# Performance work log

Hardware: AMD Instinct MI355X
Metric: run time of the kernel (lower is better)

The kernel has to match this reference:

```python
import jax, jax.numpy as jnp
import numpy as np

EPS = 1e-06

def elu_feature_map(x):
    # elu(x) + 1, matching torch.nn.functional.elu default alpha=1
    return jax.nn.elu(x) + 1.0

def setup_inputs() -> dict:
    key = jax.random.key(0)
    k1, k2, k3 = jax.random.split(key, 3)
    n, L, h, e = 4, 8192, 8, 64
    queries = jax.random.normal(k1, (n, L, h, e), dtype=jnp.float32)
    keys = jax.random.normal(k2, (n, L, h, e), dtype=jnp.float32)
    values = jax.random.normal(k3, (n, L, h, e), dtype=jnp.float32)
    return {"queries": queries, "keys": keys, "values": values}

def reference(queries, keys, values):
    n, l, h, e = queries.shape
    softmax_temp = e ** (-0.25)
    q = elu_feature_map(queries * softmax_temp)   # [n, l, h, e]
    k = elu_feature_map(keys * softmax_temp)      # [n, s, h, e]
    # kv: sum over sequence of outer products k (x) v -> [n, h, d_v, e]
    kv = jnp.einsum('nshd,nshm->nhmd', k, values)
    # normalizer z = 1 / (q . sum_s k)
    z = 1.0 / (jnp.einsum('nlhd,nhd->nlh', q, k.sum(axis=1)) + EPS)
    v = jnp.einsum('nlhd,nhmd,nlh->nlhm', q, kv, z)
    return v
```

## Files before the change

kernel.cpp:

```cpp
#include <hip/hip_runtime.h>

#define N_      4
#define L_      8192
#define H_      8
#define E_      64
#define NH_     (N_ * H_)
#define STRIDE_ (H_ * E_)
#define SPLIT_  32
#define RPB_    (L_ / SPLIT_)
#define NKB_    (RPB_ / 32)
#define PITCH_  40

#define PKV_FLOATS ((size_t)NH_ * SPLIT_ * E_ * E_)
#define PKS_FLOATS ((size_t)NH_ * SPLIT_ * E_)
#define KVT_FLOATS ((size_t)NH_ * E_ * E_ / 2)
#define PKS_OFF  PKV_FLOATS
#define KVT_OFF  (PKV_FLOATS + PKS_FLOATS)
#define KSUM_OFF (KVT_OFF + KVT_FLOATS)

typedef short bf16x8 __attribute__((ext_vector_type(8)));
typedef float f32x16 __attribute__((ext_vector_type(16)));

__device__ __forceinline__ float featmap(float x) {
    float xs = x * 0.35355339059327373f;
    return xs > 0.0f ? xs + 1.0f : __expf(xs);
}
__device__ __forceinline__ unsigned short f2bf(float f) {
    union { float f; unsigned u; } c{f};
    unsigned r = c.u + 0x7FFFu + ((c.u >> 16) & 1u);
    return (unsigned short)(r >> 16);
}
__device__ __forceinline__ unsigned pack2(float lo, float hi) {
    return (unsigned)f2bf(lo) | ((unsigned)f2bf(hi) << 16);
}

__global__ __launch_bounds__(256) void la_kv(
    const float* __restrict__ keys, const float* __restrict__ values,
    float* __restrict__ pkv, float* __restrict__ pks)
{
    const int blk = blockIdx.x;
    const int nh = blk / SPLIT_, chunk = blk % SPLIT_;
    const int n = nh / H_, h = nh % H_;
    const int t = threadIdx.x, l = t & 63;
    const int w = t >> 6, wd = w >> 1, wm = w & 1;
    const int d4 = t & 15, p = t >> 4;
    const int lm = l & 31, lh = l >> 5;

    __shared__ unsigned short Kb[2][E_][PITCH_];
    __shared__ unsigned short Vb[2][E_][PITCH_];

    f32x16 acc = {0,0,0,0,0,0,0,0,0,0,0,0,0,0,0,0};
    float sk0 = 0.f, sk1 = 0.f, sk2 = 0.f, sk3 = 0.f;

    const size_t base = (size_t)n * (L_ * H_ * E_) + (size_t)h * E_;
    const float* kp = keys   + base + (size_t)(chunk * RPB_ + 2 * p) * STRIDE_ + d4 * 4;
    const float* vp = values + base + (size_t)(chunk * RPB_ + 2 * p) * STRIDE_ + d4 * 4;

    float4 k0 = *(const float4*)kp;
    float4 k1 = *(const float4*)(kp + STRIDE_);
    float4 v0 = *(const float4*)vp;
    float4 v1 = *(const float4*)(vp + STRIDE_);

    for (int i = 0; i < NKB_; ++i) {
        const int buf = i & 1;
        float4 nk0, nk1, nv0, nv1;
        if (i + 1 < NKB_) {
            kp += 32 * STRIDE_; vp += 32 * STRIDE_;
            nk0 = *(const float4*)kp; nk1 = *(const float4*)(kp + STRIDE_);
            nv0 = *(const float4*)vp; nv1 = *(const float4*)(vp + STRIDE_);
        } else { nk0 = k0; nk1 = k1; nv0 = v0; nv1 = v1; }

        const float a0 = featmap(k0.x), a1 = featmap(k0.y),
                    a2 = featmap(k0.z), a3 = featmap(k0.w);
        const float b0 = featmap(k1.x), b1 = featmap(k1.y),
                    b2 = featmap(k1.z), b3 = featmap(k1.w);
        sk0 += a0 + b0; sk1 += a1 + b1; sk2 += a2 + b2; sk3 += a3 + b3;

        *(unsigned*)&Kb[buf][4 * d4 + 0][2 * p] = pack2(a0, b0);
        *(unsigned*)&Kb[buf][4 * d4 + 1][2 * p] = pack2(a1, b1);
        *(unsigned*)&Kb[buf][4 * d4 + 2][2 * p] = pack2(a2, b2);
        *(unsigned*)&Kb[buf][4 * d4 + 3][2 * p] = pack2(a3, b3);
        *(unsigned*)&Vb[buf][4 * d4 + 0][2 * p] = pack2(v0.x, v1.x);
        *(unsigned*)&Vb[buf][4 * d4 + 1][2 * p] = pack2(v0.y, v1.y);
        *(unsigned*)&Vb[buf][4 * d4 + 2][2 * p] = pack2(v0.z, v1.z);
        *(unsigned*)&Vb[buf][4 * d4 + 3][2 * p] = pack2(v0.w, v1.w);

        __syncthreads();

        bf16x8 af0 = *(const bf16x8*)&Kb[buf][32 * wd + lm][8 * lh];
        bf16x8 bf0 = *(const bf16x8*)&Vb[buf][32 * wm + lm][8 * lh];
        acc = __builtin_amdgcn_mfma_f32_32x32x16_bf16(af0, bf0, acc, 0, 0, 0);
        bf16x8 af1 = *(const bf16x8*)&Kb[buf][32 * wd + lm][16 + 8 * lh];
        bf16x8 bf1 = *(const bf16x8*)&Vb[buf][32 * wm + lm][16 + 8 * lh];
        acc = __builtin_amdgcn_mfma_f32_32x32x16_bf16(af1, bf1, acc, 0, 0, 0);

        k0 = nk0; k1 = nk1; v0 = nv0; v1 = nv1;
    }

    float* dst = pkv + (size_t)blk * (E_ * E_);
    #pragma unroll
    for (int r = 0; r < 16; ++r) {
        const int ro = (r & 3) + 8 * (r >> 2) + 4 * lh;
        dst[(32 * wd + ro) * E_ + 32 * wm + lm] = acc[r];
    }

    __syncthreads();
    float* ksb = (float*)&Kb[0][0][0];
    *(float4*)&ksb[p * 68 + 4 * d4] = make_float4(sk0, sk1, sk2, sk3);
    __syncthreads();
    if (t < E_) {
        float ss = 0.f;
        #pragma unroll
        for (int pp = 0; pp < 16; ++pp) ss += ksb[pp * 68 + t];
        pks[(size_t)blk * E_ + t] = ss;
    }
}

__global__ __launch_bounds__(256) void la_reduce(
    const float* __restrict__ pkv, const float* __restrict__ pks,
    unsigned short* __restrict__ kvt, float* __restrict__ ksum)
{
    const int b = blockIdx.x, nh = b >> 4, sl = b & 15;
    const int e = sl * 256 + threadIdx.x;
    const float* src = pkv + (size_t)nh * SPLIT_ * (E_ * E_) + e;
    float s = 0.f;
    #pragma unroll
    for (int c = 0; c < SPLIT_; ++c) s += src[(size_t)c * (E_ * E_)];
    const int d = e >> 6, m = e & 63;
    kvt[(size_t)nh * (E_ * E_) + m * E_ + d] = f2bf(s);

    if (sl == 0 && threadIdx.x < E_) {
        const float* sp = pks + (size_t)nh * SPLIT_ * E_ + threadIdx.x;
        float ss = 0.f;
        #pragma unroll
        for (int c = 0; c < SPLIT_; ++c) ss += sp[c * E_];
        ksum[nh * E_ + threadIdx.x] = ss;
    }
}

__global__ __launch_bounds__(256) void la_out(
    const float* __restrict__ q, const unsigned short* __restrict__ kvt,
    const float* __restrict__ ksum, float* __restrict__ out)
{
    const int blk = blockIdx.x, nh = blk >> 5, tile = blk & 31;
    const int n = nh / H_, h = nh % H_;
    const int t = threadIdx.x, l = t & 63, w = t >> 6;
    const int lm = l & 31, lh = l >> 5;

    __shared__ float zbuf[4][32];

    const unsigned short* kb = kvt + (size_t)nh * (E_ * E_);
    const float* ks = ksum + nh * E_;

    bf16x8 bfr[4][2];
    float4 kr[4][2];
    #pragma unroll
    for (int st = 0; st < 4; ++st) {
        #pragma unroll
        for (int c = 0; c < 2; ++c)
            bfr[st][c] = *(const bf16x8*)&kb[(32 * c + lm) * E_ + st * 16 + 8 * lh];
        kr[st][0] = *(const float4*)&ks[st * 16 + 8 * lh];
        kr[st][1] = *(const float4*)&ks[st * 16 + 8 * lh + 4];
    }

    const size_t base = (size_t)n * (L_ * H_ * E_) + (size_t)h * E_;

    #pragma unroll
    for (int bnd = 0; bnd < 2; ++bnd) {
        const int l0 = tile * 256 + w * 64 + bnd * 32;
        const float* qp = q + base + (size_t)(l0 + lm) * STRIDE_ + 8 * lh;

        float4 qa[4], qb[4];
        #pragma unroll
        for (int st = 0; st < 4; ++st) {
            qa[st] = *(const float4*)(qp + st * 16);
            qb[st] = *(const float4*)(qp + st * 16 + 4);
        }

        float zd = 0.f;
        bf16x8 af[4];
        #pragma unroll
        for (int st = 0; st < 4; ++st) {
            const float f0 = featmap(qa[st].x), f1 = featmap(qa[st].y),
                        f2 = featmap(qa[st].z), f3 = featmap(qa[st].w);
            const float g0 = featmap(qb[st].x), g1 = featmap(qb[st].y),
                        g2 = featmap(qb[st].z), g3 = featmap(qb[st].w);
            zd += f0 * kr[st][0].x + f1 * kr[st][0].y + f2 * kr[st][0].z + f3 * kr[st][0].w
                + g0 * kr[st][1].x + g1 * kr[st][1].y + g2 * kr[st][1].z + g3 * kr[st][1].w;
            bf16x8 a;
            a[0] = (short)f2bf(f0); a[1] = (short)f2bf(f1);
            a[2] = (short)f2bf(f2); a[3] = (short)f2bf(f3);
            a[4] = (short)f2bf(g0); a[5] = (short)f2bf(g1);
            a[6] = (short)f2bf(g2); a[7] = (short)f2bf(g3);
            af[st] = a;
        }
        zd += __shfl_xor(zd, 32);
        const float z = 1.0f / (zd + 1e-6f);
        if (l < 32) zbuf[w][l] = z;
        __builtin_amdgcn_wave_barrier();

        f32x16 c0 = {0,0,0,0,0,0,0,0,0,0,0,0,0,0,0,0};
        f32x16 c1 = {0,0,0,0,0,0,0,0,0,0,0,0,0,0,0,0};
        #pragma unroll
        for (int st = 0; st < 4; ++st) {
            c0 = __builtin_amdgcn_mfma_f32_32x32x16_bf16(af[st], bfr[st][0], c0, 0, 0, 0);
            c1 = __builtin_amdgcn_mfma_f32_32x32x16_bf16(af[st], bfr[st][1], c1, 0, 0, 0);
        }

        float* op = out + base + (size_t)l0 * STRIDE_ + lm;
        #pragma unroll
        for (int r = 0; r < 16; ++r) {
            const int ro = (r & 3) + 8 * (r >> 2) + 4 * lh;
            const float zz = zbuf[w][ro];
            op[(size_t)ro * STRIDE_]      = c0[r] * zz;
            op[(size_t)ro * STRIDE_ + 32] = c1[r] * zz;
        }
        __builtin_amdgcn_wave_barrier();
    }
}

extern "C" void kernel_launch(void* const* d_in, const int* in_sizes, int n_in,
                              void* d_out, int out_size, void* d_ws, size_t ws_size,
                              hipStream_t stream) {
    (void)in_sizes; (void)n_in; (void)out_size; (void)ws_size;
    const float* qq = (const float*)d_in[0];
    const float* kk = (const float*)d_in[1];
    const float* vv = (const float*)d_in[2];
    float* outp = (float*)d_out;
    float* ws   = (float*)d_ws;

    float* pkv = ws;
    float* pks = ws + PKS_OFF;
    unsigned short* kvt = (unsigned short*)(ws + KVT_OFF);
    float* ksm = ws + KSUM_OFF;

    la_kv<<<NH_ * SPLIT_, 256, 0, stream>>>(kk, vv, pkv, pks);
    la_reduce<<<NH_ * 16, 256, 0, stream>>>(pkv, pks, kvt, ksm);
    la_out<<<NH_ * 32, 256, 0, stream>>>(qq, kvt, ksm, outp);
}
```

Before: 66.21 us.

## Load K/V directly into MFMA operand registers, dropping LDS staging and barriers

The kv kernel no longer stages bf16-converted K and V tiles through shared memory. Each lane now loads the column elements it needs straight from global memory into registers, double-buffered one 16-row chunk ahead, and feeds MFMA from them. The key-sum reduction uses a cross-lane shuffle instead of a shared-memory pass. This removes LDS traffic and per-iteration __syncthreads. In exchange, global loads become scalar strided accesses (one float per row per lane), each wave re-reads K/V its neighbours also load, and featmap is computed redundantly across waves.

```diff
diff --git a/kernel.cpp b/kernel.cpp
--- a/kernel.cpp
+++ b/kernel.cpp
@@ -8,8 +8,7 @@
 #define STRIDE_ (H_ * E_)
 #define SPLIT_  32
 #define RPB_    (L_ / SPLIT_)
-#define NKB_    (RPB_ / 32)
-#define PITCH_  40
+#define NCH_    (RPB_ / 16)
 
 #define PKV_FLOATS ((size_t)NH_ * SPLIT_ * E_ * E_)
 #define PKS_FLOATS ((size_t)NH_ * SPLIT_ * E_)
@@ -29,9 +28,6 @@
     union { float f; unsigned u; } c{f};
     unsigned r = c.u + 0x7FFFu + ((c.u >> 16) & 1u);
     return (unsigned short)(r >> 16);
-}
-__device__ __forceinline__ unsigned pack2(float lo, float hi) {
-    return (unsigned)f2bf(lo) | ((unsigned)f2bf(hi) << 16);
 }
 
 __global__ __launch_bounds__(256) void la_kv(
@@ -43,58 +39,42 @@
     const int n = nh / H_, h = nh % H_;
     const int t = threadIdx.x, l = t & 63;
     const int w = t >> 6, wd = w >> 1, wm = w & 1;
-    const int d4 = t & 15, p = t >> 4;
     const int lm = l & 31, lh = l >> 5;
 
-    __shared__ unsigned short Kb[2][E_][PITCH_];
-    __shared__ unsigned short Vb[2][E_][PITCH_];
+    const size_t base = (size_t)n * (L_ * H_ * E_) + (size_t)h * E_;
+    const int s0 = chunk * RPB_;
+    const float* kcol = keys   + base + (size_t)s0 * STRIDE_ + 32 * wd + lm;
+    const float* vcol = values + base + (size_t)s0 * STRIDE_ + 32 * wm + lm;
 
     f32x16 acc = {0,0,0,0,0,0,0,0,0,0,0,0,0,0,0,0};
-    float sk0 = 0.f, sk1 = 0.f, sk2 = 0.f, sk3 = 0.f;
-
-    const size_t base = (size_t)n * (L_ * H_ * E_) + (size_t)h * E_;
-    const float* kp = keys   + base + (size_t)(chunk * RPB_ + 2 * p) * STRIDE_ + d4 * 4;
-    const float* vp = values + base + (size_t)(chunk * RPB_ + 2 * p) * STRIDE_ + d4 * 4;
-
-    float4 k0 = *(const float4*)kp;
-    float4 k1 = *(const float4*)(kp + STRIDE_);
-    float4 v0 = *(const float4*)vp;
-    float4 v1 = *(const float4*)(vp + STRIDE_);
-
-    for (int i = 0; i < NKB_; ++i) {
-        const int buf = i & 1;
-        float4 nk0, nk1, nv0, nv1;
-        if (i + 1 < NKB_) {
-            kp += 32 * STRIDE_; vp += 32 * STRIDE_;
-            nk0 = *(const float4*)kp; nk1 = *(const float4*)(kp + STRIDE_);
-            nv0 = *(const float4*)vp; nv1 = *(const float4*)(vp + STRIDE_);
-        } else { nk0 = k0; nk1 = k1; nv0 = v0; nv1 = v1; }
-
-        const float a0 = featmap(k0.x), a1 = featmap(k0.y),
-                    a2 = featmap(k0.z), a3 = featmap(k0.w);
-        const float b0 = featmap(k1.x), b1 = featmap(k1.y),
-                    b2 = featmap(k1.z), b3 = featmap(k1.w);
-        sk0 += a0 + b0; sk1 += a1 + b1; sk2 += a2 + b2; sk3 += a3 + b3;
-
-        *(unsigned*)&Kb[buf][4 * d4 + 0][2 * p] = pack2(a0, b0);
-        *(unsigned*)&Kb[buf][4 * d4 + 1][2 * p] = pack2(a1, b1);
-        *(unsigned*)&Kb[buf][4 * d4 + 2][2 * p] = pack2(a2, b2);
-        *(unsigned*)&Kb[buf][4 * d4 + 3][2 * p] = pack2(a3, b3);
-        *(unsigned*)&Vb[buf][4 * d4 + 0][2 * p] = pack2(v0.x, v1.x);
-        *(unsigned*)&Vb[buf][4 * d4 + 1][2 * p] = pack2(v0.y, v1.y);
-        *(unsigned*)&Vb[buf][4 * d4 + 2][2 * p] = pack2(v0.z, v1.z);
-        *(unsigned*)&Vb[buf][4 * d4 + 3][2 * p] = pack2(v0.w, v1.w);
-
-        __syncthreads();
-
-        bf16x8 af0 = *(const bf16x8*)&Kb[buf][32 * wd + lm][8 * lh];
-        bf16x8 bf0 = *(const bf16x8*)&Vb[buf][32 * wm + lm][8 * lh];
-        acc = __builtin_amdgcn_mfma_f32_32x32x16_bf16(af0, bf0, acc, 0, 0, 0);
-        bf16x8 af1 = *(const bf16x8*)&Kb[buf][32 * wd + lm][16 + 8 * lh];
-        bf16x8 bf1 = *(const bf16x8*)&Vb[buf][32 * wm + lm][16 + 8 * lh];
-        acc = __builtin_amdgcn_mfma_f32_32x32x16_bf16(af1, bf1, acc, 0, 0, 0);
-
-        k0 = nk0; k1 = nk1; v0 = nv0; v1 = nv1;
+    float ksum = 0.f;
+
+    float ka[2][8], va[2][8];
+    #pragma unroll
+    for (int j = 0; j < 8; ++j) {
+        ka[0][j] = kcol[(size_t)(8 * lh + j) * STRIDE_];
+        va[0][j] = vcol[(size_t)(8 * lh + j) * STRIDE_];
+    }
+
+    #pragma unroll
+    for (int c = 0; c < NCH_; ++c) {
+        const int cur = c & 1, nxt = cur ^ 1;
+        if (c + 1 < NCH_) {
+            #pragma unroll
+            for (int j = 0; j < 8; ++j) {
+                ka[nxt][j] = kcol[(size_t)((c + 1) * 16 + 8 * lh + j) * STRIDE_];
+                va[nxt][j] = vcol[(size_t)((c + 1) * 16 + 8 * lh + j) * STRIDE_];
+            }
+        }
+        bf16x8 af, bf;
+        #pragma unroll
+        for (int j = 0; j < 8; ++j) {
+            const float kf = featmap(ka[cur][j]);
+            ksum += kf;
+            af[j] = (short)f2bf(kf);
+            bf[j] = (short)f2bf(va[cur][j]);
+        }
+        acc = __builtin_amdgcn_mfma_f32_32x32x16_bf16(af, bf, acc, 0, 0, 0);
     }
 
     float* dst = pkv + (size_t)blk * (E_ * E_);
@@ -104,16 +84,9 @@
         dst[(32 * wd + ro) * E_ + 32 * wm + lm] = acc[r];
     }
 
-    __syncthreads();
-    float* ksb = (float*)&Kb[0][0][0];
-    *(float4*)&ksb[p * 68 + 4 * d4] = make_float4(sk0, sk1, sk2, sk3);
-    __syncthreads();
-    if (t < E_) {
-        float ss = 0.f;
-        #pragma unroll
-        for (int pp = 0; pp < 16; ++pp) ss += ksb[pp * 68 + t];
-        pks[(size_t)blk * E_ + t] = ss;
-    }
+    ksum += __shfl_xor(ksum, 32);
+    if (wm == 0 && lh == 0)
+        pks[(size_t)blk * E_ + 32 * wd + lm] = ksum;
 }
 
 __global__ __launch_bounds__(256) void la_reduce(
```

After: 68.31 us. 1.03x slower.
